# Kernel tuning notes

Measured on AMD Instinct MI355X. Metric: run time of the kernel, lower is better.

## Reference

```python
import jax, jax.numpy as jnp
import numpy as np

H = 56; W = 56; WS = 7; SHIFT = 3; HEADS = 4; DIM = 128
N = WS * WS  # 49 tokens per window
EPS = 1e-5


def _rel_pos_index():
    c = np.stack(np.meshgrid(np.arange(WS), np.arange(WS), indexing='ij')).reshape(2, -1)
    r = (c[:, :, None] - c[:, None, :]).transpose(1, 2, 0)
    r[..., 0] += WS - 1
    r[..., 1] += WS - 1
    r[..., 0] *= 2 * WS - 1
    return jnp.asarray(r.sum(-1))  # [N, N] int


def _attn_mask():
    img = np.zeros((H, W))
    sl = (slice(0, -WS), slice(-WS, -SHIFT), slice(-SHIFT, None))
    cnt = 0
    for hs in sl:
        for ws_ in sl:
            img[hs, ws_] = cnt
            cnt += 1
    mw = img.reshape(H // WS, WS, W // WS, WS).transpose(0, 2, 1, 3).reshape(-1, N)
    d = mw[:, None, :] - mw[:, :, None]  # [nW, N, N]
    return jnp.asarray(np.where(d != 0, -100.0, 0.0).astype(np.float32))


def _ln(x, w, b):
    m = x.mean(-1, keepdims=True)
    v = ((x - m) ** 2).mean(-1, keepdims=True)
    return (x - m) / jnp.sqrt(v + EPS) * w + b


def setup_inputs() -> dict:
    key = jax.random.key(0)
    ks = jax.random.split(key, 8)
    B = 64
    return {
        'x': jax.random.normal(ks[0], (B, H * W, DIM), jnp.float32),
        'qkv_w': jax.random.normal(ks[1], (DIM, 3 * DIM), jnp.float32) * 0.02,
        'qkv_b': jnp.zeros((3 * DIM,), jnp.float32),
        'proj_w': jax.random.normal(ks[2], (DIM, DIM), jnp.float32) * 0.02,
        'proj_b': jnp.zeros((DIM,), jnp.float32),
        'rpb_table': jax.random.normal(ks[3], ((2 * WS - 1) ** 2, HEADS), jnp.float32) * 0.02,
        'norm1_w': jnp.ones((DIM,), jnp.float32),
        'norm1_b': jnp.zeros((DIM,), jnp.float32),
        'norm2_w': jnp.ones((DIM,), jnp.float32),
        'norm2_b': jnp.zeros((DIM,), jnp.float32),
        'mlp_w1': jax.random.normal(ks[4], (DIM, 4 * DIM), jnp.float32) * 0.02,
        'mlp_b1': jnp.zeros((4 * DIM,), jnp.float32),
        'mlp_w2': jax.random.normal(ks[5], (4 * DIM, DIM), jnp.float32) * 0.02,
        'mlp_b2': jnp.zeros((DIM,), jnp.float32),
    }


def reference(x, qkv_w, qkv_b, proj_w, proj_b, rpb_table,
              norm1_w, norm1_b, norm2_w, norm2_b,
              mlp_w1, mlp_b1, mlp_w2, mlp_b2):
    B = x.shape[0]
    C = DIM
    hd = C // HEADS
    shortcut = x
    h = _ln(x, norm1_w, norm1_b).reshape(B, H, W, C)
    # cyclic shift
    h = jnp.roll(h, (-SHIFT, -SHIFT), axis=(1, 2))
    # window partition -> [B*nW, N, C]
    xw = h.reshape(B, H // WS, WS, W // WS, WS, C).transpose(0, 1, 3, 2, 4, 5).reshape(-1, N, C)
    qkv = (xw @ qkv_w + qkv_b).reshape(-1, N, 3, HEADS, hd).transpose(2, 0, 3, 1, 4)
    q, k, v = qkv[0] * (hd ** -0.5), qkv[1], qkv[2]  # [B*nW, heads, N, hd]
    attn = jnp.einsum('whnd,whmd->whnm', q, k)
    bias = rpb_table[_rel_pos_index().reshape(-1)].reshape(N, N, HEADS).transpose(2, 0, 1)
    attn = attn + bias[None]
    mask = _attn_mask()  # [nW, N, N]
    nW = mask.shape[0]
    attn = attn.reshape(B, nW, HEADS, N, N) + mask[None, :, None]
    attn = jax.nn.softmax(attn.reshape(-1, HEADS, N, N), axis=-1)
    out = jnp.einsum('whnm,whmd->wnhd', attn, v).reshape(-1, N, C)
    out = out @ proj_w + proj_b
    # window reverse + reverse shift
    out = out.reshape(B, H // WS, W // WS, WS, WS, C).transpose(0, 1, 3, 2, 4, 5).reshape(B, H, W, C)
    out = jnp.roll(out, (SHIFT, SHIFT), axis=(1, 2)).reshape(B, H * W, C)
    x = shortcut + out
    h2 = _ln(x, norm2_w, norm2_b)
    h2 = jax.nn.gelu(h2 @ mlp_w1 + mlp_b1, approximate=False) @ mlp_w2 + mlp_b2
    return x + h2
```

## Files before the change

kernel.cpp:

```cpp
#include <hip/hip_runtime.h>

#define HH 56
#define WW2 56
#define WS 7
#define SHIFT 3
#define HEADS 4
#define DIM 128
#define NTOK 49
#define BATCH 64
#define TOKENS (BATCH*HH*WW2)
#define NWIN 64
#define WINDOWS (BATCH*NWIN)

typedef __bf16 bf16x8 __attribute__((ext_vector_type(8)));
typedef float  f32x4  __attribute__((ext_vector_type(4)));

__device__ __forceinline__ unsigned short f2bf(float f) {
  unsigned u = __float_as_uint(f);
  u += 0x7fffu + ((u >> 16) & 1u);
  return (unsigned short)(u >> 16);
}

__device__ __forceinline__ void st4(unsigned short* p, float a, float b, float c, float d) {
  ushort4 pk; pk.x = f2bf(a); pk.y = f2bf(b); pk.z = f2bf(c); pk.w = f2bf(d);
  *(ushort4*)p = pk;
}

__device__ __forceinline__ int reg3(int g) { return g >= 53 ? 2 : (g >= 49 ? 1 : 0); }

__global__ __launch_bounds__(256) void k_prep(
    const float* __restrict__ qkv_w, const float* __restrict__ proj_w,
    const float* __restrict__ w1, const float* __restrict__ w2,
    unsigned short* __restrict__ qkvwT, unsigned short* __restrict__ projwT,
    unsigned short* __restrict__ w1T, unsigned short* __restrict__ w2T)
{
  int idx = blockIdx.x * 256 + threadIdx.x;
  if (idx < 49152) {
    int n = idx >> 7, k = idx & 127;
    qkvwT[idx] = f2bf(qkv_w[k * 384 + n]);
  } else if (idx < 65536) {
    int i = idx - 49152; int n = i >> 7, k = i & 127;
    projwT[i] = f2bf(proj_w[k * 128 + n]);
  } else if (idx < 131072) {
    int i = idx - 65536; int n = i >> 7, k = i & 127;
    w1T[i] = f2bf(w1[k * 512 + n]);
  } else {
    int i = idx - 131072; int n = i >> 9, k = i & 511;
    w2T[i] = f2bf(w2[k * 128 + n]);
  }
}

__global__ __launch_bounds__(256) void k_tbl(const float* __restrict__ rpb, float* __restrict__ tbl)
{
  int idx = blockIdx.x * 256 + threadIdx.x;
  int kt = idx & 63, qt = (idx >> 6) & 63, h = (idx >> 12) & 3, cls = idx >> 14;
  float v;
  if (qt >= NTOK || kt >= NTOK) v = -3e38f;
  else {
    int qi = qt / 7, qj = qt % 7, ki = kt / 7, kj = kt % 7;
    int bi = (cls & 2) ? 49 : 0, bj = (cls & 1) ? 49 : 0;
    int rq = reg3(bi + qi) * 3 + reg3(bj + qj);
    int rk = reg3(bi + ki) * 3 + reg3(bj + kj);
    v = rpb[((qi - ki + 6) * 13 + (qj - kj + 6)) * HEADS + h] + (rq != rk ? -100.0f : 0.0f);
  }
  tbl[idx] = v;
}

__global__ __launch_bounds__(256, 2) void k_attn(
    const float* __restrict__ x,
    const float* __restrict__ n1w, const float* __restrict__ n1b,
    const unsigned short* __restrict__ qkvwT,
    const float* __restrict__ qkv_b,
    const unsigned short* __restrict__ projwT,
    const float* __restrict__ proj_b,
    const float* __restrict__ tbl,
    unsigned short* __restrict__ attn_out)
{
  __shared__ __align__(16) unsigned short s_x[64 * 136];
  __shared__ __align__(16) unsigned short s_qk[64 * 264];
  __shared__ __align__(16) unsigned short s_vT[128 * 72];

  int tid = threadIdx.x;
  int wave = tid >> 6;
  int lane = tid & 63;
  int l = lane & 15, g = lane >> 4;
  int win = blockIdx.x;
  int wi = (win & 63) >> 3, wj = win & 7;
  int bi = win >> 6;

  {
    float2 wv1 = *(const float2*)(n1w + lane * 2);
    float2 bv1 = *(const float2*)(n1b + lane * 2);
    float2 vr[13];
    #pragma unroll
    for (int rr = 0; rr < 13; ++rr) {
      int row = wave + rr * 4;
      if (row < NTOK) {
        int ti = row / 7, tj = row % 7;
        int i = wi * WS + ti + SHIFT; if (i >= HH) i -= HH;
        int j = wj * WS + tj + SHIFT; if (j >= WW2) j -= WW2;
        const float* xp = x + ((size_t)(bi * (HH * WW2) + i * WW2 + j)) * DIM;
        vr[rr] = *(const float2*)(xp + lane * 2);
      }
    }
    #pragma unroll
    for (int rr = 0; rr < 13; ++rr) {
      int row = wave + rr * 4;
      if (row < NTOK) {
        float2 v = vr[rr];
        float s = v.x + v.y, sq = v.x * v.x + v.y * v.y;
        #pragma unroll
        for (int off = 32; off; off >>= 1) {
          s += __shfl_xor(s, off);
          sq += __shfl_xor(sq, off);
        }
        float mean = s * (1.0f / DIM);
        float var = sq * (1.0f / DIM) - mean * mean;
        float rs = rsqrtf(var + 1e-5f);
        float y0 = (v.x - mean) * rs * wv1.x + bv1.x;
        float y1 = (v.y - mean) * rs * wv1.y + bv1.y;
        unsigned pack = ((unsigned)f2bf(y1) << 16) | (unsigned)f2bf(y0);
        *(unsigned*)&s_x[row * 136 + lane * 2] = pack;
      }
    }
  }
  for (int idx = tid; idx < 15 * 17; idx += 256) {
    int row = 49 + idx / 17, seg = idx % 17;
    *(uint4*)&s_x[row * 136 + seg * 8] = make_uint4(0, 0, 0, 0);
  }
  __syncthreads();

  bf16x8 xf[4][4];
  #pragma unroll
  for (int nt = 0; nt < 4; ++nt)
    #pragma unroll
    for (int kk = 0; kk < 4; ++kk)
      xf[nt][kk] = *(const bf16x8*)&s_x[(nt * 16 + l) * 136 + kk * 32 + g * 8];

  #pragma unroll
  for (int wti = 0; wti < 6; ++wti) {
    int wt = wave * 6 + wti;
    bf16x8 wf[4];
    #pragma unroll
    for (int kk = 0; kk < 4; ++kk)
      wf[kk] = *(const bf16x8*)(qkvwT + (size_t)(wt * 16 + l) * DIM + kk * 32 + g * 8);
    f32x4 acc[4];
    #pragma unroll
    for (int nt = 0; nt < 4; ++nt) acc[nt] = (f32x4){0.f, 0.f, 0.f, 0.f};
    #pragma unroll
    for (int kk = 0; kk < 4; ++kk)
      #pragma unroll
      for (int nt = 0; nt < 4; ++nt)
        acc[nt] = __builtin_amdgcn_mfma_f32_16x16x32_bf16(wf[kk], xf[nt][kk], acc[nt], 0, 0, 0);
    float4 b4 = *(const float4*)(qkv_b + wt * 16 + g * 4);
    if (wt < 16) {
      float sc = wt < 8 ? 0.17677669529663687f : 1.0f;
      #pragma unroll
      for (int nt = 0; nt < 4; ++nt)
        st4(&s_qk[(nt * 16 + l) * 264 + wt * 16 + g * 4],
            (acc[nt][0] + b4.x) * sc, (acc[nt][1] + b4.y) * sc,
            (acc[nt][2] + b4.z) * sc, (acc[nt][3] + b4.w) * sc);
    } else {
      int d0 = wt * 16 - 256 + g * 4;
      #pragma unroll
      for (int nt = 0; nt < 4; ++nt) {
        s_vT[(d0 + 0) * 72 + nt * 16 + l] = f2bf(acc[nt][0] + b4.x);
        s_vT[(d0 + 1) * 72 + nt * 16 + l] = f2bf(acc[nt][1] + b4.y);
        s_vT[(d0 + 2) * 72 + nt * 16 + l] = f2bf(acc[nt][2] + b4.z);
        s_vT[(d0 + 3) * 72 + nt * 16 + l] = f2bf(acc[nt][3] + b4.w);
      }
    }
  }
  __syncthreads();

  int h = wave;
  bf16x8 kf[4], qf[4];
  #pragma unroll
  for (int mt = 0; mt < 4; ++mt)
    kf[mt] = *(const bf16x8*)&s_qk[(mt * 16 + l) * 264 + 128 + h * 32 + g * 8];
  #pragma unroll
  for (int nt = 0; nt < 4; ++nt)
    qf[nt] = *(const bf16x8*)&s_qk[(nt * 16 + l) * 264 + h * 32 + g * 8];
  __syncthreads();

  int clsid = ((wi == 7) ? 2 : 0) | ((wj == 7) ? 1 : 0);
  const float* tb = tbl + ((clsid * 4 + h) << 12);
  f32x4 sc[4][4];
  #pragma unroll
  for (int nt = 0; nt < 4; ++nt)
    #pragma unroll
    for (int mt = 0; mt < 4; ++mt) {
      f32x4 ci = *(const f32x4*)(tb + (nt * 16 + l) * 64 + mt * 16 + g * 4);
      sc[mt][nt] = __builtin_amdgcn_mfma_f32_16x16x32_bf16(kf[mt], qf[nt], ci, 0, 0, 0);
    }

  #pragma unroll
  for (int nt = 0; nt < 4; ++nt) {
    float m = sc[0][nt][0];
    #pragma unroll
    for (int mt = 0; mt < 4; ++mt)
      #pragma unroll
      for (int rr = 0; rr < 4; ++rr) m = fmaxf(m, sc[mt][nt][rr]);
    m = fmaxf(m, __shfl_xor(m, 16));
    m = fmaxf(m, __shfl_xor(m, 32));
    float ssum = 0.f;
    #pragma unroll
    for (int mt = 0; mt < 4; ++mt)
      #pragma unroll
      for (int rr = 0; rr < 4; ++rr) {
        float e = __expf(sc[mt][nt][rr] - m);
        sc[mt][nt][rr] = e;
        ssum += e;
      }
    ssum += __shfl_xor(ssum, 16);
    ssum += __shfl_xor(ssum, 32);
    float inv = 1.0f / ssum;
    #pragma unroll
    for (int mt = 0; mt < 4; ++mt)
      st4(&s_qk[(nt * 16 + l) * 264 + h * 64 + mt * 16 + g * 4],
          sc[mt][nt][0] * inv, sc[mt][nt][1] * inv, sc[mt][nt][2] * inv, sc[mt][nt][3] * inv);
  }

  bf16x8 vf[2][2], pf[4][2];
  #pragma unroll
  for (int dt = 0; dt < 2; ++dt)
    #pragma unroll
    for (int kk = 0; kk < 2; ++kk)
      vf[dt][kk] = *(const bf16x8*)&s_vT[(h * 32 + dt * 16 + l) * 72 + kk * 32 + g * 8];
  #pragma unroll
  for (int nt = 0; nt < 4; ++nt)
    #pragma unroll
    for (int kk = 0; kk < 2; ++kk)
      pf[nt][kk] = *(const bf16x8*)&s_qk[(nt * 16 + l) * 264 + h * 64 + kk * 32 + g * 8];
  #pragma unroll
  for (int dt = 0; dt < 2; ++dt)
    #pragma unroll
    for (int nt = 0; nt < 4; ++nt) {
      f32x4 a = (f32x4){0.f, 0.f, 0.f, 0.f};
      a = __builtin_amdgcn_mfma_f32_16x16x32_bf16(vf[dt][0], pf[nt][0], a, 0, 0, 0);
      a = __builtin_amdgcn_mfma_f32_16x16x32_bf16(vf[dt][1], pf[nt][1], a, 0, 0, 0);
      st4(&s_x[(nt * 16 + l) * 136 + h * 32 + dt * 16 + g * 4], a[0], a[1], a[2], a[3]);
    }
  __syncthreads();

  unsigned short* stage = s_vT;
  bf16x8 of[4][4];
  #pragma unroll
  for (int nt = 0; nt < 4; ++nt)
    #pragma unroll
    for (int kk = 0; kk < 4; ++kk)
      of[nt][kk] = *(const bf16x8*)&s_x[(nt * 16 + l) * 136 + kk * 32 + g * 8];
  #pragma unroll
  for (int wti = 0; wti < 2; ++wti) {
    int wt = wave * 2 + wti;
    bf16x8 wf[4];
    #pragma unroll
    for (int kk = 0; kk < 4; ++kk)
      wf[kk] = *(const bf16x8*)(projwT + (size_t)(wt * 16 + l) * DIM + kk * 32 + g * 8);
    f32x4 acc[4];
    #pragma unroll
    for (int nt = 0; nt < 4; ++nt) acc[nt] = (f32x4){0.f, 0.f, 0.f, 0.f};
    #pragma unroll
    for (int kk = 0; kk < 4; ++kk)
      #pragma unroll
      for (int nt = 0; nt < 4; ++nt)
        acc[nt] = __builtin_amdgcn_mfma_f32_16x16x32_bf16(wf[kk], of[nt][kk], acc[nt], 0, 0, 0);
    float4 b4 = *(const float4*)(proj_b + wt * 16 + g * 4);
    #pragma unroll
    for (int nt = 0; nt < 4; ++nt)
      st4(&stage[(nt * 16 + l) * 136 + wt * 16 + g * 4],
          acc[nt][0] + b4.x, acc[nt][1] + b4.y, acc[nt][2] + b4.z, acc[nt][3] + b4.w);
  }
  __syncthreads();

  unsigned short* outp = attn_out + (size_t)win * (NTOK * DIM);
  for (int idx = tid; idx < NTOK * 16; idx += 256) {
    int row = idx >> 4, seg = idx & 15;
    *(uint4*)(outp + idx * 8) = *(const uint4*)&stage[row * 136 + seg * 8];
  }
}

__device__ __forceinline__ float gelu_f(float x) {
  float x2 = x * x;
  float t = x * __builtin_fmaf(x2, -0.10294429f, -2.3022077f);
  float e = __builtin_amdgcn_exp2f(t);
  return x * __builtin_amdgcn_rcpf(1.0f + e);
}

__global__ __launch_bounds__(256) void k_mlp(
    const float* __restrict__ x, const unsigned short* __restrict__ attn,
    const float* __restrict__ n2w, const float* __restrict__ n2b,
    const unsigned short* __restrict__ w1T, const float* __restrict__ b1,
    const unsigned short* __restrict__ w2T, const float* __restrict__ b2,
    float* __restrict__ io)
{
  __shared__ __align__(16) unsigned short s_t[2][64 * 136];
  __shared__ float s_part[64][4][2];
  int tid = threadIdx.x;
  int wave = tid >> 6;
  int lane = tid & 63;
  int l = lane & 15, g = lane >> 4;
  size_t m0 = (size_t)blockIdx.x * 64;
  int col0 = wave * 32 + g * 4;

  float4 xz[4][2];
  float sA[4], sQ[4];
  #pragma unroll
  for (int nt = 0; nt < 4; ++nt) {
    int row = nt * 16 + l;
    int t = (int)m0 + row;
    int bi = t / (HH * WW2);
    int r = t % (HH * WW2);
    int i = r / WW2, j = r % WW2;
    int si = i >= SHIFT ? i - SHIFT : i + (HH - SHIFT);
    int sj = j >= SHIFT ? j - SHIFT : j + (WW2 - SHIFT);
    int win = bi * NWIN + (si / WS) * 8 + (sj / WS);
    int tok = (si % WS) * WS + (sj % WS);
    const float* xp = x + (size_t)t * DIM;
    const unsigned short* ap = attn + ((size_t)(win * NTOK + tok)) * DIM;
    float s = 0.f, sq = 0.f;
    #pragma unroll
    for (int wti = 0; wti < 2; ++wti) {
      int col = col0 + wti * 16;
      float4 xv = *(const float4*)(xp + col);
      ushort4 av = *(const ushort4*)(ap + col);
      float4 z;
      z.x = xv.x + __uint_as_float((unsigned)av.x << 16);
      z.y = xv.y + __uint_as_float((unsigned)av.y << 16);
      z.z = xv.z + __uint_as_float((unsigned)av.z << 16);
      z.w = xv.w + __uint_as_float((unsigned)av.w << 16);
      xz[nt][wti] = z;
      s += z.x + z.y + z.z + z.w;
      sq += z.x * z.x + z.y * z.y + z.z * z.z + z.w * z.w;
    }
    s += __shfl_xor(s, 16); s += __shfl_xor(s, 32);
    sq += __shfl_xor(sq, 16); sq += __shfl_xor(sq, 32);
    sA[nt] = s; sQ[nt] = sq;
  }
  if (g == 0) {
    #pragma unroll
    for (int nt = 0; nt < 4; ++nt) {
      s_part[nt * 16 + l][wave][0] = sA[nt];
      s_part[nt * 16 + l][wave][1] = sQ[nt];
    }
  }
  __syncthreads();
  float4 wv0 = *(const float4*)(n2w + col0);
  float4 wv1 = *(const float4*)(n2w + col0 + 16);
  float4 bv0 = *(const float4*)(n2b + col0);
  float4 bv1 = *(const float4*)(n2b + col0 + 16);
  #pragma unroll
  for (int nt = 0; nt < 4; ++nt) {
    int row = nt * 16 + l;
    float s = 0.f, sq = 0.f;
    #pragma unroll
    for (int wv = 0; wv < 4; ++wv) { s += s_part[row][wv][0]; sq += s_part[row][wv][1]; }
    float mean = s * (1.0f / DIM);
    float var = sq * (1.0f / DIM) - mean * mean;
    float rs = rsqrtf(var + 1e-5f);
    float4 z0 = xz[nt][0], z1 = xz[nt][1];
    st4(&s_t[1][row * 136 + col0],
        (z0.x - mean) * rs * wv0.x + bv0.x, (z0.y - mean) * rs * wv0.y + bv0.y,
        (z0.z - mean) * rs * wv0.z + bv0.z, (z0.w - mean) * rs * wv0.w + bv0.w);
    st4(&s_t[1][row * 136 + col0 + 16],
        (z1.x - mean) * rs * wv1.x + bv1.x, (z1.y - mean) * rs * wv1.y + bv1.y,
        (z1.z - mean) * rs * wv1.z + bv1.z, (z1.w - mean) * rs * wv1.w + bv1.w);
  }
  __syncthreads();

  bf16x8 hf[4][4];
  #pragma unroll
  for (int nt = 0; nt < 4; ++nt)
    #pragma unroll
    for (int kk = 0; kk < 4; ++kk)
      hf[nt][kk] = *(const bf16x8*)&s_t[1][(nt * 16 + l) * 136 + kk * 32 + g * 8];

  f32x4 o[2][4];
  #pragma unroll
  for (int wti = 0; wti < 2; ++wti)
    #pragma unroll
    for (int nt = 0; nt < 4; ++nt) o[wti][nt] = (f32x4){0.f, 0.f, 0.f, 0.f};

  for (int c = 0; c < 4; ++c) {
    unsigned short* buf = s_t[c & 1];
    #pragma unroll
    for (int wti = 0; wti < 2; ++wti) {
      int wt = wave * 2 + wti;
      int n0 = c * 128 + wt * 16;
      bf16x8 wf[4];
      #pragma unroll
      for (int kk = 0; kk < 4; ++kk)
        wf[kk] = *(const bf16x8*)(w1T + (size_t)(n0 + l) * DIM + kk * 32 + g * 8);
      f32x4 acc[4];
      #pragma unroll
      for (int nt = 0; nt < 4; ++nt) acc[nt] = (f32x4){0.f, 0.f, 0.f, 0.f};
      #pragma unroll
      for (int kk = 0; kk < 4; ++kk)
        #pragma unroll
        for (int nt = 0; nt < 4; ++nt)
          acc[nt] = __builtin_amdgcn_mfma_f32_16x16x32_bf16(wf[kk], hf[nt][kk], acc[nt], 0, 0, 0);
      float4 b4 = *(const float4*)(b1 + n0 + g * 4);
      #pragma unroll
      for (int nt = 0; nt < 4; ++nt)
        st4(&buf[(nt * 16 + l) * 136 + wt * 16 + g * 4],
            gelu_f(acc[nt][0] + b4.x), gelu_f(acc[nt][1] + b4.y),
            gelu_f(acc[nt][2] + b4.z), gelu_f(acc[nt][3] + b4.w));
    }
    __syncthreads();
    #pragma unroll
    for (int kk = 0; kk < 4; ++kk) {
      bf16x8 tf[4];
      #pragma unroll
      for (int nt = 0; nt < 4; ++nt)
        tf[nt] = *(const bf16x8*)&buf[(nt * 16 + l) * 136 + kk * 32 + g * 8];
      #pragma unroll
      for (int wti = 0; wti < 2; ++wti) {
        int wt = wave * 2 + wti;
        bf16x8 wf2 = *(const bf16x8*)(w2T + (size_t)(wt * 16 + l) * 512 + c * 128 + kk * 32 + g * 8);
        #pragma unroll
        for (int nt = 0; nt < 4; ++nt)
          o[wti][nt] = __builtin_amdgcn_mfma_f32_16x16x32_bf16(wf2, tf[nt], o[wti][nt], 0, 0, 0);
      }
    }
  }

  #pragma unroll
  for (int wti = 0; wti < 2; ++wti) {
    int wt = wave * 2 + wti;
    float4 b4 = *(const float4*)(b2 + wt * 16 + g * 4);
    #pragma unroll
    for (int nt = 0; nt < 4; ++nt) {
      float4 z = xz[nt][wti];
      float4 pv;
      pv.x = z.x + o[wti][nt][0] + b4.x;
      pv.y = z.y + o[wti][nt][1] + b4.y;
      pv.z = z.z + o[wti][nt][2] + b4.z;
      pv.w = z.w + o[wti][nt][3] + b4.w;
      *(float4*)(io + (m0 + nt * 16 + l) * DIM + wt * 16 + g * 4) = pv;
    }
  }
}

extern "C" void kernel_launch(void* const* d_in, const int* in_sizes, int n_in,
                              void* d_out, int out_size, void* d_ws, size_t ws_size,
                              hipStream_t stream) {
  const float* x       = (const float*)d_in[0];
  const float* qkv_w   = (const float*)d_in[1];
  const float* qkv_b   = (const float*)d_in[2];
  const float* proj_w  = (const float*)d_in[3];
  const float* proj_b  = (const float*)d_in[4];
  const float* rpb     = (const float*)d_in[5];
  const float* n1w     = (const float*)d_in[6];
  const float* n1b     = (const float*)d_in[7];
  const float* n2w     = (const float*)d_in[8];
  const float* n2b     = (const float*)d_in[9];
  const float* mlp_w1  = (const float*)d_in[10];
  const float* mlp_b1  = (const float*)d_in[11];
  const float* mlp_w2  = (const float*)d_in[12];
  const float* mlp_b2  = (const float*)d_in[13];
  float* out = (float*)d_out;

  char* ws = (char*)d_ws;
  const size_t TOKB = (size_t)TOKENS * DIM * 2;
  unsigned short* attn_o = (unsigned short*)(ws);
  unsigned short* qkvwT  = (unsigned short*)(ws + TOKB);
  unsigned short* projwT = (unsigned short*)(ws + TOKB + 98304);
  unsigned short* w1T    = (unsigned short*)(ws + TOKB + 98304 + 32768);
  unsigned short* w2T    = (unsigned short*)(ws + TOKB + 98304 + 32768 + 131072);
  float*          tbl    = (float*)(ws + TOKB + 98304 + 32768 + 131072 + 131072);

  k_prep<<<768, 256, 0, stream>>>(qkv_w, proj_w, mlp_w1, mlp_w2, qkvwT, projwT, w1T, w2T);
  k_tbl<<<256, 256, 0, stream>>>(rpb, tbl);
  k_attn<<<WINDOWS, 256, 0, stream>>>(x, n1w, n1b, qkvwT, qkv_b, projwT, proj_b, tbl, attn_o);
  k_mlp<<<TOKENS / 64, 256, 0, stream>>>(x, attn_o, n2w, n2b, w1T, mlp_b1, w2T, mlp_b2, out);
}
```

Baseline: 465.9 us.

## Use 8 waves per attention block and hoist MLP w2 fragment loads

The attention kernel now launches 512 threads per window. Work is split over eight waves: half the rows in LayerNorm, three QKV tiles per wave, each head split across two waves by query tiles for softmax and by d-tiles for PV, and one proj tile per wave. An extra barrier is added because the PV step now reads probabilities written by the sibling wave. In the MLP kernel, the w2 weight fragments for each chunk are loaded into registers up front, before the GELU stage, to hide global latency. The trade is more parallelism per window against register pressure under launch_bounds(512,4) and an extra sync.

```diff
diff --git a/kernel.cpp b/kernel.cpp
--- a/kernel.cpp
+++ b/kernel.cpp
@@ -66,7 +66,7 @@
   tbl[idx] = v;
 }
 
-__global__ __launch_bounds__(256, 2) void k_attn(
+__global__ __launch_bounds__(512, 4) void k_attn(
     const float* __restrict__ x,
     const float* __restrict__ n1w, const float* __restrict__ n1b,
     const unsigned short* __restrict__ qkvwT,
@@ -91,10 +91,10 @@
   {
     float2 wv1 = *(const float2*)(n1w + lane * 2);
     float2 bv1 = *(const float2*)(n1b + lane * 2);
-    float2 vr[13];
-    #pragma unroll
-    for (int rr = 0; rr < 13; ++rr) {
-      int row = wave + rr * 4;
+    float2 vr[7];
+    #pragma unroll
+    for (int rr = 0; rr < 7; ++rr) {
+      int row = wave + rr * 8;
       if (row < NTOK) {
         int ti = row / 7, tj = row % 7;
         int i = wi * WS + ti + SHIFT; if (i >= HH) i -= HH;
@@ -104,8 +104,8 @@
       }
     }
     #pragma unroll
-    for (int rr = 0; rr < 13; ++rr) {
-      int row = wave + rr * 4;
+    for (int rr = 0; rr < 7; ++rr) {
+      int row = wave + rr * 8;
       if (row < NTOK) {
         float2 v = vr[rr];
         float s = v.x + v.y, sq = v.x * v.x + v.y * v.y;
@@ -124,7 +124,7 @@
       }
     }
   }
-  for (int idx = tid; idx < 15 * 17; idx += 256) {
+  for (int idx = tid; idx < 15 * 17; idx += 512) {
     int row = 49 + idx / 17, seg = idx % 17;
     *(uint4*)&s_x[row * 136 + seg * 8] = make_uint4(0, 0, 0, 0);
   }
@@ -138,8 +138,8 @@
       xf[nt][kk] = *(const bf16x8*)&s_x[(nt * 16 + l) * 136 + kk * 32 + g * 8];
 
   #pragma unroll
-  for (int wti = 0; wti < 6; ++wti) {
-    int wt = wave * 6 + wti;
+  for (int wti = 0; wti < 3; ++wti) {
+    int wt = wave * 3 + wti;
     bf16x8 wf[4];
     #pragma unroll
     for (int kk = 0; kk < 4; ++kk)
@@ -173,34 +173,39 @@
   }
   __syncthreads();
 
-  int h = wave;
-  bf16x8 kf[4], qf[4];
+  int h = wave >> 1, qh = wave & 1;
+  bf16x8 kf[4], qf[2];
   #pragma unroll
   for (int mt = 0; mt < 4; ++mt)
     kf[mt] = *(const bf16x8*)&s_qk[(mt * 16 + l) * 264 + 128 + h * 32 + g * 8];
   #pragma unroll
-  for (int nt = 0; nt < 4; ++nt)
-    qf[nt] = *(const bf16x8*)&s_qk[(nt * 16 + l) * 264 + h * 32 + g * 8];
+  for (int nt2 = 0; nt2 < 2; ++nt2) {
+    int nt = qh * 2 + nt2;
+    qf[nt2] = *(const bf16x8*)&s_qk[(nt * 16 + l) * 264 + h * 32 + g * 8];
+  }
   __syncthreads();
 
   int clsid = ((wi == 7) ? 2 : 0) | ((wj == 7) ? 1 : 0);
   const float* tb = tbl + ((clsid * 4 + h) << 12);
-  f32x4 sc[4][4];
-  #pragma unroll
-  for (int nt = 0; nt < 4; ++nt)
+  f32x4 sc[4][2];
+  #pragma unroll
+  for (int nt2 = 0; nt2 < 2; ++nt2) {
+    int nt = qh * 2 + nt2;
     #pragma unroll
     for (int mt = 0; mt < 4; ++mt) {
       f32x4 ci = *(const f32x4*)(tb + (nt * 16 + l) * 64 + mt * 16 + g * 4);
-      sc[mt][nt] = __builtin_amdgcn_mfma_f32_16x16x32_bf16(kf[mt], qf[nt], ci, 0, 0, 0);
-    }
-
-  #pragma unroll
-  for (int nt = 0; nt < 4; ++nt) {
-    float m = sc[0][nt][0];
+      sc[mt][nt2] = __builtin_amdgcn_mfma_f32_16x16x32_bf16(kf[mt], qf[nt2], ci, 0, 0, 0);
+    }
+  }
+
+  #pragma unroll
+  for (int nt2 = 0; nt2 < 2; ++nt2) {
+    int nt = qh * 2 + nt2;
+    float m = sc[0][nt2][0];
     #pragma unroll
     for (int mt = 0; mt < 4; ++mt)
       #pragma unroll
-      for (int rr = 0; rr < 4; ++rr) m = fmaxf(m, sc[mt][nt][rr]);
+      for (int rr = 0; rr < 4; ++rr) m = fmaxf(m, sc[mt][nt2][rr]);
     m = fmaxf(m, __shfl_xor(m, 16));
     m = fmaxf(m, __shfl_xor(m, 32));
     float ssum = 0.f;
@@ -208,8 +213,8 @@
     for (int mt = 0; mt < 4; ++mt)
       #pragma unroll
       for (int rr = 0; rr < 4; ++rr) {
-        float e = __expf(sc[mt][nt][rr] - m);
-        sc[mt][nt][rr] = e;
+        float e = __expf(sc[mt][nt2][rr] - m);
+        sc[mt][nt2][rr] = e;
         ssum += e;
       }
     ssum += __shfl_xor(ssum, 16);
@@ -218,29 +223,27 @@
     #pragma unroll
     for (int mt = 0; mt < 4; ++mt)
       st4(&s_qk[(nt * 16 + l) * 264 + h * 64 + mt * 16 + g * 4],
-          sc[mt][nt][0] * inv, sc[mt][nt][1] * inv, sc[mt][nt][2] * inv, sc[mt][nt][3] * inv);
-  }
-
-  bf16x8 vf[2][2], pf[4][2];
-  #pragma unroll
-  for (int dt = 0; dt < 2; ++dt)
-    #pragma unroll
-    for (int kk = 0; kk < 2; ++kk)
-      vf[dt][kk] = *(const bf16x8*)&s_vT[(h * 32 + dt * 16 + l) * 72 + kk * 32 + g * 8];
+          sc[mt][nt2][0] * inv, sc[mt][nt2][1] * inv, sc[mt][nt2][2] * inv, sc[mt][nt2][3] * inv);
+  }
+  __syncthreads();
+
+  int dt = qh;
+  bf16x8 vf[2], pf[4][2];
+  #pragma unroll
+  for (int kk = 0; kk < 2; ++kk)
+    vf[kk] = *(const bf16x8*)&s_vT[(h * 32 + dt * 16 + l) * 72 + kk * 32 + g * 8];
   #pragma unroll
   for (int nt = 0; nt < 4; ++nt)
     #pragma unroll
     for (int kk = 0; kk < 2; ++kk)
       pf[nt][kk] = *(const bf16x8*)&s_qk[(nt * 16 + l) * 264 + h * 64 + kk * 32 + g * 8];
   #pragma unroll
-  for (int dt = 0; dt < 2; ++dt)
-    #pragma unroll
-    for (int nt = 0; nt < 4; ++nt) {
-      f32x4 a = (f32x4){0.f, 0.f, 0.f, 0.f};
-      a = __builtin_amdgcn_mfma_f32_16x16x32_bf16(vf[dt][0], pf[nt][0], a, 0, 0, 0);
-      a = __builtin_amdgcn_mfma_f32_16x16x32_bf16(vf[dt][1], pf[nt][1], a, 0, 0, 0);
-      st4(&s_x[(nt * 16 + l) * 136 + h * 32 + dt * 16 + g * 4], a[0], a[1], a[2], a[3]);
-    }
+  for (int nt = 0; nt < 4; ++nt) {
+    f32x4 a = (f32x4){0.f, 0.f, 0.f, 0.f};
+    a = __builtin_amdgcn_mfma_f32_16x16x32_bf16(vf[0], pf[nt][0], a, 0, 0, 0);
+    a = __builtin_amdgcn_mfma_f32_16x16x32_bf16(vf[1], pf[nt][1], a, 0, 0, 0);
+    st4(&s_x[(nt * 16 + l) * 136 + h * 32 + dt * 16 + g * 4], a[0], a[1], a[2], a[3]);
+  }
   __syncthreads();
 
   unsigned short* stage = s_vT;
@@ -250,9 +253,8 @@
     #pragma unroll
     for (int kk = 0; kk < 4; ++kk)
       of[nt][kk] = *(const bf16x8*)&s_x[(nt * 16 + l) * 136 + kk * 32 + g * 8];
-  #pragma unroll
-  for (int wti = 0; wti < 2; ++wti) {
-    int wt = wave * 2 + wti;
+  {
+    int wt = wave;
     bf16x8 wf[4];
     #pragma unroll
     for (int kk = 0; kk < 4; ++kk)
@@ -274,7 +276,7 @@
   __syncthreads();
 
   unsigned short* outp = attn_out + (size_t)win * (NTOK * DIM);
-  for (int idx = tid; idx < NTOK * 16; idx += 256) {
+  for (int idx = tid; idx < NTOK * 16; idx += 512) {
     int row = idx >> 4, seg = idx & 15;
     *(uint4*)(outp + idx * 8) = *(const uint4*)&stage[row * 136 + seg * 8];
   }
@@ -383,6 +385,12 @@
 
   for (int c = 0; c < 4; ++c) {
     unsigned short* buf = s_t[c & 1];
+    bf16x8 wf2r[2][4];
+    #pragma unroll
+    for (int wti = 0; wti < 2; ++wti)
+      #pragma unroll
+      for (int kk = 0; kk < 4; ++kk)
+        wf2r[wti][kk] = *(const bf16x8*)(w2T + (size_t)((wave * 2 + wti) * 16 + l) * 512 + c * 128 + kk * 32 + g * 8);
     #pragma unroll
     for (int wti = 0; wti < 2; ++wti) {
       int wt = wave * 2 + wti;
@@ -414,13 +422,10 @@
       for (int nt = 0; nt < 4; ++nt)
         tf[nt] = *(const bf16x8*)&buf[(nt * 16 + l) * 136 + kk * 32 + g * 8];
       #pragma unroll
-      for (int wti = 0; wti < 2; ++wti) {
-        int wt = wave * 2 + wti;
-        bf16x8 wf2 = *(const bf16x8*)(w2T + (size_t)(wt * 16 + l) * 512 + c * 128 + kk * 32 + g * 8);
+      for (int wti = 0; wti < 2; ++wti)
         #pragma unroll
         for (int nt = 0; nt < 4; ++nt)
-          o[wti][nt] = __builtin_amdgcn_mfma_f32_16x16x32_bf16(wf2, tf[nt], o[wti][nt], 0, 0, 0);
-      }
+          o[wti][nt] = __builtin_amdgcn_mfma_f32_16x16x32_bf16(wf2r[wti][kk], tf[nt], o[wti][nt], 0, 0, 0);
     }
   }
 
@@ -471,6 +476,6 @@
 
   k_prep<<<768, 256, 0, stream>>>(qkv_w, proj_w, mlp_w1, mlp_w2, qkvwT, projwT, w1T, w2T);
   k_tbl<<<256, 256, 0, stream>>>(rpb, tbl);
-  k_attn<<<WINDOWS, 256, 0, stream>>>(x, n1w, n1b, qkvwT, qkv_b, projwT, proj_b, tbl, attn_o);
+  k_attn<<<WINDOWS, 512, 0, stream>>>(x, n1w, n1b, qkvwT, qkv_b, projwT, proj_b, tbl, attn_o);
   k_mlp<<<TOKENS / 64, 256, 0, stream>>>(x, attn_o, n2w, n2b, w1T, mlp_b1, w2T, mlp_b2, out);
 }
```

New measurement: 462.9 us. Within noise of the previous version (-0.6%).
